# Performance work log

Measured on AMD Instinct MI355X. Metric: run time of the kernel, lower is better.

## Reference

```python
import jax, jax.numpy as jnp
import numpy as np

LMAX = 4  # number of l blocks (lmax+1 in the original)
# segment ids mapping the L2 = sum(2l+1) = 16 spherical components to their l block
SEG = np.repeat(np.arange(LMAX), 2 * np.arange(LMAX) + 1)  # [16]
SEG_ONEHOT = np.eye(LMAX, dtype=np.float32)[SEG]  # [16, LMAX]


def setup_inputs() -> dict:
    key = jax.random.key(0)
    ks = jax.random.split(key, 10)
    b, m, f, k, L2 = 16, 64, 128, 64, 16
    def rnd(kk, shape, scale):
        return jax.random.normal(kk, shape, dtype=jnp.float32) * scale
    return {
        'x': rnd(ks[0], (b, m, f, L2), 1.0),
        'y': rnd(ks[1], (b, m, f, L2), 1.0),
        'wx0': rnd(ks[2], (k, f, f, LMAX), 1.0 / np.sqrt(f * f * LMAX)),
        'wy0': rnd(ks[3], (k, f, f, LMAX), 1.0 / np.sqrt(f * f * LMAX)),
        'wx_mlp': rnd(ks[4], (2, k, k), 1.0 / np.sqrt(k)),
        'bx_mlp': rnd(ks[5], (2, k, k), 0.02),
        'wy_mlp': rnd(ks[6], (2, k, k), 1.0 / np.sqrt(k)),
        'by_mlp': rnd(ks[7], (2, k, k), 0.02),
        'wxf': rnd(ks[8], (LMAX, f, k), 1.0 / np.sqrt(k)),
        'wyf': rnd(ks[9], (LMAX, f, k), 1.0 / np.sqrt(k)),
    }


def reference(x, y, wx0, wy0, wx_mlp, bx_mlp, wy_mlp, by_mlp, wxf, wyf):
    act = jax.nn.silu
    S = jnp.asarray(SEG_ONEHOT)  # [L2, lmax]
    # outer product of y and x features, segment-summed over each l block:
    # mix[b,m,fy,fx,l] = sum_c y[b,m,fy,c] * x[b,m,fx,c] * S[c,l]
    mix = jnp.einsum('bmfc,bmgc,cl->bmfgl', y, x, S)  # [b,m,f,f,lmax]
    mx = jnp.einsum('bmfgl,kfgl->bmk', mix, wx0)
    my = jnp.einsum('bmfgl,kfgl->bmk', mix, wy0)
    for i in range(wx_mlp.shape[0]):  # the n_mlp-1 used MLP stages
        mx = act(jnp.einsum('bmk,kl->bml', mx, wx_mlp[i]) + bx_mlp[i])
        my = act(jnp.einsum('bmk,kl->bml', my, wy_mlp[i]) + by_mlp[i])
    mx = act(jnp.einsum('bmk,lfk->bmfl', mx, wxf))  # [b,m,f,lmax]
    my = act(jnp.einsum('bmk,lfk->bmfl', my, wyf))
    # broadcast each l gate over its 2l+1 components (repeat == gather by SEG)
    seg = jnp.asarray(SEG)
    res = mx[..., seg] * x + my[..., seg] * y  # [b,m,f,L2]
    return res
```

## Files before the change

kernel.cpp:

```cpp
#include <hip/hip_runtime.h>
#include <stdint.h>


#define AS1 __attribute__((address_space(1)))
#define AS3 __attribute__((address_space(3)))

typedef __bf16 bf16x8 __attribute__((ext_vector_type(8)));
typedef float f32x4 __attribute__((ext_vector_type(4)));

__device__ __forceinline__ uint16_t f2b(float f) {
  uint32_t u = __float_as_uint(f);
  u += 0x7fffu + ((u >> 16) & 1u);
  return (uint16_t)(u >> 16);
}

#if __has_builtin(__builtin_amdgcn_fdot2_f32_bf16)
typedef __bf16 bf16x2 __attribute__((ext_vector_type(2)));
__device__ __forceinline__ float dot2b(uint32_t a, uint32_t b, float c) {
  union { uint32_t u; bf16x2 v; } ua, ub;
  ua.u = a; ub.u = b;
  return __builtin_amdgcn_fdot2_f32_bf16(ua.v, ub.v, c, false);
}
#else
__device__ __forceinline__ float dot2b(uint32_t a, uint32_t b, float c) {
  float a0 = __uint_as_float(a << 16), a1 = __uint_as_float(a & 0xffff0000u);
  float b0 = __uint_as_float(b << 16), b1 = __uint_as_float(b & 0xffff0000u);
  return c + a0 * b0 + a1 * b1;
}
#endif

__global__ __launch_bounds__(256) void convert_all(
    const float* __restrict__ wx0, const float* __restrict__ wy0,
    const float* __restrict__ x, const float* __restrict__ y,
    const float* __restrict__ wxf, const float* __restrict__ wyf,
    uint16_t* __restrict__ Wb2, uint16_t* __restrict__ xb,
    uint16_t* __restrict__ yb, float* __restrict__ wfT) {
  int bid = blockIdx.x, tid = threadIdx.x;
  if (bid < 4096) {
    size_t idx = ((size_t)bid * 256 + tid) * 8;
    int side = idx >= 4194304 ? 1 : 0;
    size_t rem = side ? idx - 4194304 : idx;
    const float* src = (side ? wy0 : wx0) + rem;
    float4 v0 = *(const float4*)src;
    float4 v1 = *(const float4*)(src + 4);
    int fx0 = (int)((rem >> 2) & 127);
    int fy  = (int)((rem >> 9) & 127);
    int k   = (int)(rem >> 16);
    int n = side * 64 + k;
    int fb = fx0 >> 3;
    int slot = (fx0 >> 1) & 3;
    int pos = slot ^ ((n >> 1) & 3);
    uint32_t o0 = (uint32_t)f2b(v0.x) | ((uint32_t)f2b(v0.y) << 16);
    uint32_t o1 = (uint32_t)f2b(v0.z) | ((uint32_t)f2b(v0.w) << 16);
    uint32_t o2 = (uint32_t)f2b(v1.x) | ((uint32_t)f2b(v1.y) << 16);
    uint32_t o3 = (uint32_t)f2b(v1.z) | ((uint32_t)f2b(v1.w) << 16);
    size_t chunk = (((size_t)(fb * 128 + fy)) * 128 + n) * 4 + pos;
    *(uint4*)(Wb2 + chunk * 8) = make_uint4(o0, o1, o2, o3);
    return;
  }
  if (bid >= 6144) {
    int base = (bid - 6144) * 2048 + tid * 8;
#pragma unroll
    for (int ii = 0; ii < 8; ++ii) {
      int idx = base + ii;
      int side = idx >> 15, rem = idx & 32767;
      int k = rem >> 9, l = (rem >> 7) & 3, f = rem & 127;
      const float* src = side ? wyf : wxf;
      wfT[idx] = src[((size_t)l * 128 + f) * 64 + k];
    }
    return;
  }
  size_t i = ((size_t)(bid - 4096) * 256 + tid) * 8;
  const float* s; uint16_t* d;
  if (i < 2097152) { s = x + i;             d = xb + i; }
  else             { s = y + (i - 2097152); d = yb + (i - 2097152); }
  float4 v0 = *(const float4*)s;
  float4 v1 = *(const float4*)(s + 4);
  uint32_t o0 = (uint32_t)f2b(v0.x) | ((uint32_t)f2b(v0.y) << 16);
  uint32_t o1 = (uint32_t)f2b(v0.z) | ((uint32_t)f2b(v0.w) << 16);
  uint32_t o2 = (uint32_t)f2b(v1.x) | ((uint32_t)f2b(v1.y) << 16);
  uint32_t o3 = (uint32_t)f2b(v1.z) | ((uint32_t)f2b(v1.w) << 16);
  *(uint4*)d = make_uint4(o0, o1, o2, o3);
}

__device__ __forceinline__ void gload_lds16(const void* g, void* l) {
  __builtin_amdgcn_global_load_lds((const AS1 uint32_t*)g, (AS3 uint32_t*)l, 16, 0, 0);
}

#define PIPE_BAR(N) \
  asm volatile("s_waitcnt vmcnt(" #N ") lgkmcnt(0)\n\ts_barrier" ::: "memory")

__global__ __launch_bounds__(256, 4) void fused_gemm(
    const uint16_t* __restrict__ xb, const uint16_t* __restrict__ yb,
    const uint16_t* __restrict__ Wb2, float* __restrict__ Cpart) {
  __shared__ __align__(16) uint16_t sB[3][128 * 32];
  __shared__ __align__(16) uint16_t yS[3][1024];

  int tid = threadIdx.x;
  int w = tid >> 6, lane = tid & 63;
  int g_id = blockIdx.x;
  int fb = g_id >> 2, fyg = g_id & 3;
  int FB = fb * 8;
  int fy0 = fyg * 32;
  int m0 = blockIdx.y * 64;
  int r = lane & 15, q = lane >> 4;
  int wm = w >> 1, wn = w & 1;

  uint32_t xreg[2][16];
#pragma unroll
  for (int i = 0; i < 2; ++i) {
    const uint16_t* xp0 =
        xb + (size_t)(m0 + wm * 32 + i * 16 + r) * 2048 + (FB + 2 * q) * 16;
#pragma unroll
    for (int j2 = 0; j2 < 4; ++j2) {
      uint4 v = *(const uint4*)(xp0 + j2 * 8);
      xreg[i][j2 * 4 + 0] = v.x; xreg[i][j2 * 4 + 1] = v.y;
      xreg[i][j2 * 4 + 2] = v.z; xreg[i][j2 * 4 + 3] = v.w;
    }
  }

  f32x4 zero = {0.f, 0.f, 0.f, 0.f};
  f32x4 acc[2][4];
#pragma unroll
  for (int i = 0; i < 2; ++i)
#pragma unroll
    for (int j = 0; j < 4; ++j) acc[i][j] = zero;

  int fbfy = fb * 128 + fy0;
  auto issueB = [&](uint16_t* dstB, int t) {
    size_t base = (size_t)(fbfy + t) * 4096;
    gload_lds16(Wb2 + base + (size_t)(w * 2) * 512 + lane * 8,
                dstB + (w * 2) * 512);
    gload_lds16(Wb2 + base + (size_t)(w * 2 + 1) * 512 + lane * 8,
                dstB + (w * 2 + 1) * 512);
  };
  const uint16_t* ysrc = yb + (size_t)(m0 + lane) * 2048 + w * 8;
  auto issueY = [&](uint16_t* dstY, int t) {
    if (w < 2) gload_lds16(ysrc + (size_t)(fy0 + t) * 16, dstY + w * 512);
  };

  issueB(sB[0], 0); issueY(yS[0], 0);
  issueB(sB[1], 1); issueY(yS[1], 1);
  if (w < 2) PIPE_BAR(3); else PIPE_BAR(2);

  uint16_t *pB0 = sB[0], *pB1 = sB[1], *pB2 = sB[2];
  uint16_t *pY0 = yS[0], *pY1 = yS[1], *pY2 = yS[2];

  for (int t = 0; t < 32; ++t) {
    if (t <= 29) { issueB(pB2, t + 2); issueY(pY2, t + 2); }

    bf16x8 b[4];
#pragma unroll
    for (int j = 0; j < 4; ++j) {
      int row = wn * 64 + j * 16 + r;
      int pos = q ^ ((row >> 1) & 3);
      b[j] = *(const bf16x8*)&pB0[row * 32 + pos * 8];
    }
    uint32_t yw[2][8];
#pragma unroll
    for (int i = 0; i < 2; ++i) {
      int row = wm * 32 + i * 16 + r;
      uint4 a0 = *(const uint4*)&pY0[row * 8];
      uint4 a1 = *(const uint4*)&pY0[512 + row * 8];
      yw[i][0] = a0.x; yw[i][1] = a0.y; yw[i][2] = a0.z; yw[i][3] = a0.w;
      yw[i][4] = a1.x; yw[i][5] = a1.y; yw[i][6] = a1.z; yw[i][7] = a1.w;
    }

#pragma unroll
    for (int i = 0; i < 2; ++i) {
      uint32_t yl0 = yw[i][0] & 0xffffu, yh0 = yw[i][0] & 0xffff0000u;
      uint32_t yl4 = yw[i][4] & 0xffffu, yh4 = yw[i][4] & 0xffff0000u;
      union { uint32_t u[4]; bf16x8 v; } af;
#pragma unroll
      for (int fxp = 0; fxp < 2; ++fxp) {
        const uint32_t* xp = &xreg[i][fxp * 8];
        float g0 = dot2b(xp[0], yl0, 0.f);
        float g1 = dot2b(xp[1], yw[i][1], dot2b(xp[0], yh0, 0.f));
        float g2 = dot2b(xp[4], yl4,
                    dot2b(xp[3], yw[i][3], dot2b(xp[2], yw[i][2], 0.f)));
        float g3 = dot2b(xp[7], yw[i][7], dot2b(xp[6], yw[i][6],
                    dot2b(xp[5], yw[i][5], dot2b(xp[4], yh4, 0.f))));
        af.u[fxp * 2 + 0] = (__float_as_uint(g0) >> 16) |
                            (__float_as_uint(g1) & 0xffff0000u);
        af.u[fxp * 2 + 1] = (__float_as_uint(g2) >> 16) |
                            (__float_as_uint(g3) & 0xffff0000u);
      }
      __builtin_amdgcn_s_setprio(1);
#pragma unroll
      for (int j = 0; j < 4; ++j)
        acc[i][j] = __builtin_amdgcn_mfma_f32_16x16x32_bf16(af.v, b[j],
                                                            acc[i][j], 0, 0, 0);
      __builtin_amdgcn_s_setprio(0);
    }

    if (t <= 29)      { if (w < 2) PIPE_BAR(3); else PIPE_BAR(2); }
    else if (t == 30) PIPE_BAR(0);

    uint16_t* tp;
    tp = pB0; pB0 = pB1; pB1 = pB2; pB2 = tp;
    tp = pY0; pY0 = pY1; pY1 = pY2; pY2 = tp;
  }

  float* cbase = Cpart + (size_t)g_id * 131072;
#pragma unroll
  for (int i = 0; i < 2; ++i)
#pragma unroll
    for (int j = 0; j < 4; ++j)
#pragma unroll
      for (int reg = 0; reg < 4; ++reg) {
        int mm = m0 + wm * 32 + i * 16 + q * 4 + reg;
        int nn = wn * 64 + j * 16 + r;
        cbase[(size_t)mm * 128 + nn] = acc[i][j][reg];
      }
}

__global__ __launch_bounds__(256) void finish_kernel(
    const float* __restrict__ x, const float* __restrict__ y,
    const float* __restrict__ wx_mlp, const float* __restrict__ bx_mlp,
    const float* __restrict__ wy_mlp, const float* __restrict__ by_mlp,
    const float* __restrict__ wfT,
    const float* __restrict__ Cpart, float* __restrict__ out) {
  const int seg[16] = {0,1,1,1,2,2,2,2,2,3,3,3,3,3,3,3};
  __shared__ float sred[256];
  __shared__ float sm[128];
  __shared__ float sg[2][128][4];
  int t = threadIdx.x;
  int bm = blockIdx.x;
  int mi = bm & 63;

  {
    int col = t & 127, hh = t >> 7;
    const float* cp = Cpart + (size_t)(hh * 32) * 131072 + (size_t)bm * 128 + col;
    float s = 0.f;
#pragma unroll 8
    for (int sp = 0; sp < 32; ++sp)
      s += cp[(size_t)sp * 131072];
    sred[t] = s;
  }
  __syncthreads();
  if (t < 128) sm[t] = sred[t] + sred[t + 128];
  __syncthreads();

  for (int st = 0; st < 2; ++st) {
    float v = 0.f;
    if (t < 128) {
      int side = t >> 6, j = t & 63;
      const float* wmlp = side ? wy_mlp : wx_mlp;
      const float* bmlp = side ? by_mlp : bx_mlp;
      const float* mv = sm + side * 64;
#pragma unroll 8
      for (int k = 0; k < 64; ++k)
        v += mv[k] * wmlp[(st * 64 + k) * 64 + j];
      v += bmlp[(st * 64 + mi) * 64 + j];
      v = v / (1.f + __expf(-v));
    }
    __syncthreads();
    if (t < 128) sm[t] = v;
    __syncthreads();
  }

  {
    int side = t >> 7, f = t & 127;
    const float* base = wfT + side * 32768;
    const float* mv = sm + side * 64;
    float gg[4] = {0.f, 0.f, 0.f, 0.f};
#pragma unroll 8
    for (int k = 0; k < 64; ++k) {
      float m2 = mv[k];
#pragma unroll
      for (int l = 0; l < 4; ++l)
        gg[l] += m2 * base[(k * 4 + l) * 128 + f];
    }
#pragma unroll
    for (int l = 0; l < 4; ++l)
      sg[side][f][l] = gg[l] / (1.f + __expf(-gg[l]));
  }
  __syncthreads();

  {
    int f = t >> 1, half = t & 1;
    size_t base = ((size_t)bm * 128 + f) * 16 + half * 8;
    float4 xa = *(const float4*)(x + base), xb4 = *(const float4*)(x + base + 4);
    float4 ya = *(const float4*)(y + base), yb4 = *(const float4*)(y + base + 4);
    float xv[8] = {xa.x, xa.y, xa.z, xa.w, xb4.x, xb4.y, xb4.z, xb4.w};
    float yv[8] = {ya.x, ya.y, ya.z, ya.w, yb4.x, yb4.y, yb4.z, yb4.w};
    float o[8];
#pragma unroll
    for (int ii = 0; ii < 8; ++ii) {
      int c = half * 8 + ii;
      o[ii] = sg[0][f][seg[c]] * xv[ii] + sg[1][f][seg[c]] * yv[ii];
    }
    *(float4*)(out + base)     = make_float4(o[0], o[1], o[2], o[3]);
    *(float4*)(out + base + 4) = make_float4(o[4], o[5], o[6], o[7]);
  }
}

extern "C" void kernel_launch(void* const* d_in, const int* in_sizes, int n_in,
                              void* d_out, int out_size, void* d_ws, size_t ws_size,
                              hipStream_t stream) {
  const float* x      = (const float*)d_in[0];
  const float* y      = (const float*)d_in[1];
  const float* wx0    = (const float*)d_in[2];
  const float* wy0    = (const float*)d_in[3];
  const float* wx_mlp = (const float*)d_in[4];
  const float* bx_mlp = (const float*)d_in[5];
  const float* wy_mlp = (const float*)d_in[6];
  const float* by_mlp = (const float*)d_in[7];
  const float* wxf    = (const float*)d_in[8];
  const float* wyf    = (const float*)d_in[9];
  float* out = (float*)d_out;

  uint16_t* Wb2   = (uint16_t*)d_ws;
  uint16_t* xb    = (uint16_t*)((char*)d_ws + (size_t)16777216);
  uint16_t* yb    = (uint16_t*)((char*)d_ws + (size_t)20971520);
  float*    Cpart = (float*)((char*)d_ws + (size_t)25165824);
  float*    wfT   = (float*)((char*)d_ws + (size_t)58720256);

  convert_all<<<6176, 256, 0, stream>>>(wx0, wy0, x, y, wxf, wyf, Wb2, xb, yb, wfT);
  fused_gemm<<<dim3(64, 16), 256, 0, stream>>>(xb, yb, Wb2, Cpart);
  finish_kernel<<<1024, 256, 0, stream>>>(x, y, wx_mlp, bx_mlp, wy_mlp, by_mlp,
                                          wfT, Cpart, out);
}
```

Measured before the change: 171.9 us.

## Keep full weight slab resident in LDS and stream only y per wave

The GEMM now launches 512-thread blocks, each of which loads its entire 128KB weight slab (one fb/fy-group, one of the x/y output halves) into LDS once. It then loops over 512 rows, with each wave handling two 32-row m tiles in sequence, and streams only y through per-wave triple buffers with no block-wide barriers inside the loop. The y tensor is pre-transposed into an fy-major layout and the weight layout is re-swizzled to match. This removes the repeated global weight traffic per 64-row tile and the per-step block barriers. In exchange, the large LDS footprint limits occupancy, the launch has only 256 blocks, and the waitcnt accounting is fragile.

```diff
diff --git a/kernel.cpp b/kernel.cpp
--- a/kernel.cpp
+++ b/kernel.cpp
@@ -34,28 +34,29 @@
     const float* __restrict__ x, const float* __restrict__ y,
     const float* __restrict__ wxf, const float* __restrict__ wyf,
     uint16_t* __restrict__ Wb2, uint16_t* __restrict__ xb,
-    uint16_t* __restrict__ yb, float* __restrict__ wfT) {
+    uint16_t* __restrict__ ybT, float* __restrict__ wfT) {
   int bid = blockIdx.x, tid = threadIdx.x;
   if (bid < 4096) {
-    size_t idx = ((size_t)bid * 256 + tid) * 8;
-    int side = idx >= 4194304 ? 1 : 0;
-    size_t rem = side ? idx - 4194304 : idx;
-    const float* src = (side ? wy0 : wx0) + rem;
+    int c = bid * 256 + tid;
+    int side = c >= 524288 ? 1 : 0;
+    int us = c & 524287;
+    int fxh = us & 63;
+    int t1 = us >> 6;
+    int fy = t1 & 127;
+    int k = t1 >> 7;
+    int fb = fxh >> 2, q = fxh & 3;
+    int fyg = fy >> 5, fyl = fy & 31;
+    int slab = ((fb << 2) + fyg) * 2 + side;
+    int u = ((fyl << 2) + q) ^ (k & 31);
+    size_t dsth = (size_t)slab * 65536 + (size_t)(u >> 3) * 4096 + k * 64 + (u & 7) * 8;
+    const float* src = (side ? wy0 : wx0) + (size_t)us * 8;
     float4 v0 = *(const float4*)src;
     float4 v1 = *(const float4*)(src + 4);
-    int fx0 = (int)((rem >> 2) & 127);
-    int fy  = (int)((rem >> 9) & 127);
-    int k   = (int)(rem >> 16);
-    int n = side * 64 + k;
-    int fb = fx0 >> 3;
-    int slot = (fx0 >> 1) & 3;
-    int pos = slot ^ ((n >> 1) & 3);
     uint32_t o0 = (uint32_t)f2b(v0.x) | ((uint32_t)f2b(v0.y) << 16);
     uint32_t o1 = (uint32_t)f2b(v0.z) | ((uint32_t)f2b(v0.w) << 16);
     uint32_t o2 = (uint32_t)f2b(v1.x) | ((uint32_t)f2b(v1.y) << 16);
     uint32_t o3 = (uint32_t)f2b(v1.z) | ((uint32_t)f2b(v1.w) << 16);
-    size_t chunk = (((size_t)(fb * 128 + fy)) * 128 + n) * 4 + pos;
-    *(uint4*)(Wb2 + chunk * 8) = make_uint4(o0, o1, o2, o3);
+    *(uint4*)(Wb2 + dsth) = make_uint4(o0, o1, o2, o3);
     return;
   }
   if (bid >= 6144) {
@@ -70,148 +71,190 @@
     }
     return;
   }
-  size_t i = ((size_t)(bid - 4096) * 256 + tid) * 8;
-  const float* s; uint16_t* d;
-  if (i < 2097152) { s = x + i;             d = xb + i; }
-  else             { s = y + (i - 2097152); d = yb + (i - 2097152); }
-  float4 v0 = *(const float4*)s;
-  float4 v1 = *(const float4*)(s + 4);
-  uint32_t o0 = (uint32_t)f2b(v0.x) | ((uint32_t)f2b(v0.y) << 16);
-  uint32_t o1 = (uint32_t)f2b(v0.z) | ((uint32_t)f2b(v0.w) << 16);
-  uint32_t o2 = (uint32_t)f2b(v1.x) | ((uint32_t)f2b(v1.y) << 16);
-  uint32_t o3 = (uint32_t)f2b(v1.z) | ((uint32_t)f2b(v1.w) << 16);
-  *(uint4*)d = make_uint4(o0, o1, o2, o3);
+  if (bid < 5120) {
+    size_t i = ((size_t)(bid - 4096) * 256 + tid) * 8;
+    const float* s = x + i;
+    float4 v0 = *(const float4*)s;
+    float4 v1 = *(const float4*)(s + 4);
+    uint32_t o0 = (uint32_t)f2b(v0.x) | ((uint32_t)f2b(v0.y) << 16);
+    uint32_t o1 = (uint32_t)f2b(v0.z) | ((uint32_t)f2b(v0.w) << 16);
+    uint32_t o2 = (uint32_t)f2b(v1.x) | ((uint32_t)f2b(v1.y) << 16);
+    uint32_t o3 = (uint32_t)f2b(v1.z) | ((uint32_t)f2b(v1.w) << 16);
+    *(uint4*)(xb + i) = make_uint4(o0, o1, o2, o3);
+    return;
+  }
+  {
+    int c = (bid - 5120) * 256 + tid;
+    int half = c & 1, fy = (c >> 1) & 127, m = c >> 8;
+    const float* s = y + (size_t)c * 8;
+    float4 v0 = *(const float4*)s;
+    float4 v1 = *(const float4*)(s + 4);
+    uint32_t o0 = (uint32_t)f2b(v0.x) | ((uint32_t)f2b(v0.y) << 16);
+    uint32_t o1 = (uint32_t)f2b(v0.z) | ((uint32_t)f2b(v0.w) << 16);
+    uint32_t o2 = (uint32_t)f2b(v1.x) | ((uint32_t)f2b(v1.y) << 16);
+    uint32_t o3 = (uint32_t)f2b(v1.z) | ((uint32_t)f2b(v1.w) << 16);
+    *(uint4*)(ybT + ((size_t)fy * 1024 + m) * 16 + half * 8) =
+        make_uint4(o0, o1, o2, o3);
+  }
 }
 
 __device__ __forceinline__ void gload_lds16(const void* g, void* l) {
   __builtin_amdgcn_global_load_lds((const AS1 uint32_t*)g, (AS3 uint32_t*)l, 16, 0, 0);
 }
 
-#define PIPE_BAR(N) \
-  asm volatile("s_waitcnt vmcnt(" #N ") lgkmcnt(0)\n\ts_barrier" ::: "memory")
-
-__global__ __launch_bounds__(256, 4) void fused_gemm(
-    const uint16_t* __restrict__ xb, const uint16_t* __restrict__ yb,
+#define SB0 __builtin_amdgcn_sched_barrier(0)
+#define SFENCE asm volatile("" ::: "memory")
+#define VMW(N) asm volatile("s_waitcnt vmcnt(" #N ")" ::: "memory")
+
+#define YDMA(BUF, FF)                                                         \
+  gload_lds16(ybT + ((size_t)(fy0 + (FF)) * 1024 + mbase + (lane >> 1)) * 16  \
+                  + (lane & 1) * 8,                                           \
+              ySw + (BUF) * 512)
+
+#define STEP(CUR, FF, VMN, DOY)                                               \
+  do {                                                                        \
+    SB0;           \
+    if (DOY) YDMA(((CUR) + 2) % 3, (FF) + 2);                                 \
+    VMW(VMN);                                                                 \
+    SB0;              \
+    const uint16_t* yrow = ySw + (CUR) * 512;                                 \
+    uint32_t yw[2][8];                                                        \
+    _Pragma("unroll") for (int i_ = 0; i_ < 2; ++i_) {                        \
+      const uint16_t* bp_ = yrow + (i_ * 16 + r) * 16;                        \
+      uint4 a0_ = *(const uint4*)bp_;                                         \
+      uint4 a1_ = *(const uint4*)(bp_ + 8);                                   \
+      yw[i_][0] = a0_.x; yw[i_][1] = a0_.y; yw[i_][2] = a0_.z; yw[i_][3] = a0_.w; \
+      yw[i_][4] = a1_.x; yw[i_][5] = a1_.y; yw[i_][6] = a1_.z; yw[i_][7] = a1_.w; \
+    }                                                                         \
+    bf16x8 bfr[4];                                                            \
+    _Pragma("unroll") for (int j_ = 0; j_ < 4; ++j_) {                        \
+      int rowb_ = j_ * 16 + r;                                                \
+      int u_ = (((FF) << 2) + q) ^ (rowb_ & 31);                              \
+      bfr[j_] = *(const bf16x8*)&sB[(u_ >> 3) * 4096 + rowb_ * 64 + (u_ & 7) * 8]; \
+    }                                                                         \
+    _Pragma("unroll") for (int i_ = 0; i_ < 2; ++i_) {                        \
+      uint32_t yl0 = yw[i_][0] & 0xffffu, yh0 = yw[i_][0] & 0xffff0000u;      \
+      uint32_t yl4 = yw[i_][4] & 0xffffu, yh4 = yw[i_][4] & 0xffff0000u;      \
+      union { uint32_t u[4]; bf16x8 v; } af;                                  \
+      _Pragma("unroll") for (int fxp = 0; fxp < 2; ++fxp) {                   \
+        const uint32_t* xp = &xreg[i_][fxp * 8];                              \
+        float g0 = dot2b(xp[0], yl0, 0.f);                                    \
+        float g1 = dot2b(xp[1], yw[i_][1], dot2b(xp[0], yh0, 0.f));           \
+        float g2 = dot2b(xp[4], yl4,                                          \
+                    dot2b(xp[3], yw[i_][3], dot2b(xp[2], yw[i_][2], 0.f)));   \
+        float g3 = dot2b(xp[7], yw[i_][7], dot2b(xp[6], yw[i_][6],            \
+                    dot2b(xp[5], yw[i_][5], dot2b(xp[4], yh4, 0.f))));        \
+        af.u[fxp * 2 + 0] = (__float_as_uint(g0) >> 16) |                     \
+                            (__float_as_uint(g1) & 0xffff0000u);              \
+        af.u[fxp * 2 + 1] = (__float_as_uint(g2) >> 16) |                     \
+                            (__float_as_uint(g3) & 0xffff0000u);              \
+      }                                                                       \
+      _Pragma("unroll") for (int j_ = 0; j_ < 4; ++j_)                        \
+        acc[i_][j_] = __builtin_amdgcn_mfma_f32_16x16x32_bf16(af.v, bfr[j_],  \
+                                                              acc[i_][j_], 0, 0, 0); \
+    }                                                                         \
+  } while (0)
+
+__global__ __launch_bounds__(512, 2) void fused_gemm(
+    const uint16_t* __restrict__ xb, const uint16_t* __restrict__ ybT,
     const uint16_t* __restrict__ Wb2, float* __restrict__ Cpart) {
-  __shared__ __align__(16) uint16_t sB[3][128 * 32];
-  __shared__ __align__(16) uint16_t yS[3][1024];
-
-  int tid = threadIdx.x;
-  int w = tid >> 6, lane = tid & 63;
-  int g_id = blockIdx.x;
-  int fb = g_id >> 2, fyg = g_id & 3;
-  int FB = fb * 8;
-  int fy0 = fyg * 32;
-  int m0 = blockIdx.y * 64;
+  __shared__ __align__(16) uint16_t sB[65536];
+  __shared__ __align__(16) uint16_t yS[12288];
+
+  int tid = threadIdx.x, w = tid >> 6, lane = tid & 63;
+  int slab = blockIdx.x, kkg = slab >> 1, nhalf = slab & 1;
+  int fb = kkg >> 2, fyg = kkg & 3;
+  int FB = fb * 8, fy0 = fyg * 32;
+  int m0 = blockIdx.y * 512;
   int r = lane & 15, q = lane >> 4;
-  int wm = w >> 1, wn = w & 1;
+  uint16_t* ySw = yS + w * 1536;
+  int mbase = m0 + w * 64;
 
   uint32_t xreg[2][16];
-#pragma unroll
-  for (int i = 0; i < 2; ++i) {
-    const uint16_t* xp0 =
-        xb + (size_t)(m0 + wm * 32 + i * 16 + r) * 2048 + (FB + 2 * q) * 16;
-#pragma unroll
-    for (int j2 = 0; j2 < 4; ++j2) {
-      uint4 v = *(const uint4*)(xp0 + j2 * 8);
-      xreg[i][j2 * 4 + 0] = v.x; xreg[i][j2 * 4 + 1] = v.y;
-      xreg[i][j2 * 4 + 2] = v.z; xreg[i][j2 * 4 + 3] = v.w;
-    }
-  }
-
+  auto loadX = [&]() {
+#pragma unroll
+    for (int i = 0; i < 2; ++i) {
+      const uint16_t* xp0 =
+          xb + (size_t)(mbase + i * 16 + r) * 2048 + (FB + 2 * q) * 16;
+#pragma unroll
+      for (int j2 = 0; j2 < 4; ++j2) {
+        uint4 v = *(const uint4*)(xp0 + j2 * 8);
+        xreg[i][j2 * 4 + 0] = v.x; xreg[i][j2 * 4 + 1] = v.y;
+        xreg[i][j2 * 4 + 2] = v.z; xreg[i][j2 * 4 + 3] = v.w;
+      }
+    }
+  };
+
+  f32x4 acc[2][4];
   f32x4 zero = {0.f, 0.f, 0.f, 0.f};
-  f32x4 acc[2][4];
 #pragma unroll
   for (int i = 0; i < 2; ++i)
 #pragma unroll
     for (int j = 0; j < 4; ++j) acc[i][j] = zero;
 
-  int fbfy = fb * 128 + fy0;
-  auto issueB = [&](uint16_t* dstB, int t) {
-    size_t base = (size_t)(fbfy + t) * 4096;
-    gload_lds16(Wb2 + base + (size_t)(w * 2) * 512 + lane * 8,
-                dstB + (w * 2) * 512);
-    gload_lds16(Wb2 + base + (size_t)(w * 2 + 1) * 512 + lane * 8,
-                dstB + (w * 2 + 1) * 512);
+  auto storeC = [&](int mb) {
+    float* cb = Cpart + (size_t)kkg * 131072;
+#pragma unroll
+    for (int i = 0; i < 2; ++i)
+#pragma unroll
+      for (int j = 0; j < 4; ++j)
+#pragma unroll
+        for (int reg = 0; reg < 4; ++reg) {
+          int mm = mb + i * 16 + q * 4 + reg;
+          int nn = nhalf * 64 + j * 16 + r;
+          cb[(size_t)mm * 128 + nn] = acc[i][j][reg];
+        }
   };
-  const uint16_t* ysrc = yb + (size_t)(m0 + lane) * 2048 + w * 8;
-  auto issueY = [&](uint16_t* dstY, int t) {
-    if (w < 2) gload_lds16(ysrc + (size_t)(fy0 + t) * 16, dstY + w * 512);
-  };
-
-  issueB(sB[0], 0); issueY(yS[0], 0);
-  issueB(sB[1], 1); issueY(yS[1], 1);
-  if (w < 2) PIPE_BAR(3); else PIPE_BAR(2);
-
-  uint16_t *pB0 = sB[0], *pB1 = sB[1], *pB2 = sB[2];
-  uint16_t *pY0 = yS[0], *pY1 = yS[1], *pY2 = yS[2];
-
-  for (int t = 0; t < 32; ++t) {
-    if (t <= 29) { issueB(pB2, t + 2); issueY(pY2, t + 2); }
-
-    bf16x8 b[4];
-#pragma unroll
-    for (int j = 0; j < 4; ++j) {
-      int row = wn * 64 + j * 16 + r;
-      int pos = q ^ ((row >> 1) & 3);
-      b[j] = *(const bf16x8*)&pB0[row * 32 + pos * 8];
-    }
-    uint32_t yw[2][8];
-#pragma unroll
-    for (int i = 0; i < 2; ++i) {
-      int row = wm * 32 + i * 16 + r;
-      uint4 a0 = *(const uint4*)&pY0[row * 8];
-      uint4 a1 = *(const uint4*)&pY0[512 + row * 8];
-      yw[i][0] = a0.x; yw[i][1] = a0.y; yw[i][2] = a0.z; yw[i][3] = a0.w;
-      yw[i][4] = a1.x; yw[i][5] = a1.y; yw[i][6] = a1.z; yw[i][7] = a1.w;
-    }
-
-#pragma unroll
-    for (int i = 0; i < 2; ++i) {
-      uint32_t yl0 = yw[i][0] & 0xffffu, yh0 = yw[i][0] & 0xffff0000u;
-      uint32_t yl4 = yw[i][4] & 0xffffu, yh4 = yw[i][4] & 0xffff0000u;
-      union { uint32_t u[4]; bf16x8 v; } af;
-#pragma unroll
-      for (int fxp = 0; fxp < 2; ++fxp) {
-        const uint32_t* xp = &xreg[i][fxp * 8];
-        float g0 = dot2b(xp[0], yl0, 0.f);
-        float g1 = dot2b(xp[1], yw[i][1], dot2b(xp[0], yh0, 0.f));
-        float g2 = dot2b(xp[4], yl4,
-                    dot2b(xp[3], yw[i][3], dot2b(xp[2], yw[i][2], 0.f)));
-        float g3 = dot2b(xp[7], yw[i][7], dot2b(xp[6], yw[i][6],
-                    dot2b(xp[5], yw[i][5], dot2b(xp[4], yh4, 0.f))));
-        af.u[fxp * 2 + 0] = (__float_as_uint(g0) >> 16) |
-                            (__float_as_uint(g1) & 0xffff0000u);
-        af.u[fxp * 2 + 1] = (__float_as_uint(g2) >> 16) |
-                            (__float_as_uint(g3) & 0xffff0000u);
-      }
-      __builtin_amdgcn_s_setprio(1);
-#pragma unroll
-      for (int j = 0; j < 4; ++j)
-        acc[i][j] = __builtin_amdgcn_mfma_f32_16x16x32_bf16(af.v, b[j],
-                                                            acc[i][j], 0, 0, 0);
-      __builtin_amdgcn_s_setprio(0);
-    }
-
-    if (t <= 29)      { if (w < 2) PIPE_BAR(3); else PIPE_BAR(2); }
-    else if (t == 30) PIPE_BAR(0);
-
-    uint16_t* tp;
-    tp = pB0; pB0 = pB1; pB1 = pB2; pB2 = tp;
-    tp = pY0; pY0 = pY1; pY1 = pY2; pY2 = tp;
-  }
-
-  float* cbase = Cpart + (size_t)g_id * 131072;
+
+  loadX();
+  SB0; SFENCE;
+  const uint16_t* wsrc = Wb2 + (size_t)slab * 65536;
+#pragma unroll
+  for (int p = 0; p < 16; ++p)
+    gload_lds16(wsrc + (size_t)p * 4096 + w * 512 + lane * 8,
+                sB + p * 4096 + w * 512);
+  SB0; SFENCE;
+  YDMA(0, 0);
+  YDMA(1, 1);
+  SB0;
+  VMW(2);
+  SB0;
+  __builtin_amdgcn_s_barrier();
+
+  for (int ft = 0; ft < 30; ft += 3) {
+    STEP(0, ft + 0, 2, true);
+    STEP(1, ft + 1, 2, true);
+    STEP(2, ft + 2, 2, true);
+  }
+  STEP(0, 30, 1, false);
+  STEP(1, 31, 0, false);
+
+  int m_st0 = mbase;
+  mbase += 32;
+  SB0;
+  loadX();
+  SB0; SFENCE;
+  YDMA(0, 0);
+  YDMA(1, 1);
+  SB0; SFENCE;
+  storeC(m_st0);
+  SB0;
 #pragma unroll
   for (int i = 0; i < 2; ++i)
 #pragma unroll
-    for (int j = 0; j < 4; ++j)
-#pragma unroll
-      for (int reg = 0; reg < 4; ++reg) {
-        int mm = m0 + wm * 32 + i * 16 + q * 4 + reg;
-        int nn = wn * 64 + j * 16 + r;
-        cbase[(size_t)mm * 128 + nn] = acc[i][j][reg];
-      }
+    for (int j = 0; j < 4; ++j) acc[i][j] = zero;
+
+  STEP(0, 0, 10, true);
+  STEP(1, 1, 10, true);
+  for (int ft = 2; ft < 29; ft += 3) {
+    STEP(2, ft + 0, 2, true);
+    STEP(0, ft + 1, 2, true);
+    STEP(1, ft + 2, 2, true);
+  }
+  STEP(2, 29, 2, true);
+  STEP(0, 30, 1, false);
+  STEP(1, 31, 0, false);
+  storeC(mbase);
 }
 
 __global__ __launch_bounds__(256) void finish_kernel(
@@ -312,12 +355,12 @@
 
   uint16_t* Wb2   = (uint16_t*)d_ws;
   uint16_t* xb    = (uint16_t*)((char*)d_ws + (size_t)16777216);
-  uint16_t* yb    = (uint16_t*)((char*)d_ws + (size_t)20971520);
+  uint16_t* ybT   = (uint16_t*)((char*)d_ws + (size_t)20971520);
   float*    Cpart = (float*)((char*)d_ws + (size_t)25165824);
   float*    wfT   = (float*)((char*)d_ws + (size_t)58720256);
 
-  convert_all<<<6176, 256, 0, stream>>>(wx0, wy0, x, y, wxf, wyf, Wb2, xb, yb, wfT);
-  fused_gemm<<<dim3(64, 16), 256, 0, stream>>>(xb, yb, Wb2, Cpart);
+  convert_all<<<6176, 256, 0, stream>>>(wx0, wy0, x, y, wxf, wyf, Wb2, xb, ybT, wfT);
+  fused_gemm<<<dim3(128, 2), 512, 0, stream>>>(xb, ybT, Wb2, Cpart);
   finish_kernel<<<1024, 256, 0, stream>>>(x, y, wx_mlp, bx_mlp, wy_mlp, by_mlp,
                                           wfT, Cpart, out);
 }
```

Result: slower. 180.9 us (+5.2%).
